# Optimization experiments

Measured on AMD Instinct MI355X. Metric: run time of the kernel, lower is better.

The kernel has to match this reference:

```python
import jax, jax.numpy as jnp
import numpy as np

N_QUBITS = 10
N_GEN = 4
Q_DEPTH = 6
BATCH = 1024


def _cz_chain_diag(n):
    # Diagonal of the CZ chain CZ(0,1) CZ(1,2) ... CZ(n-2,n-1):
    # phase (-1)^(# adjacent 1-1 pairs) per computational basis state.
    idx = np.arange(2 ** n)
    bits = (idx[:, None] >> np.arange(n - 1, -1, -1)) & 1  # wire 0 = most significant (PennyLane)
    pairs = (bits[:, :-1] & bits[:, 1:]).sum(axis=1)
    return ((-1.0) ** pairs).astype(np.float32).reshape((2,) * n)

_CZ = jnp.asarray(_cz_chain_diag(N_QUBITS))


def _ry(t):
    c = jnp.cos(0.5 * t)
    s = jnp.sin(0.5 * t)
    return jnp.stack([jnp.stack([c, -s]), jnp.stack([s, c])]).astype(jnp.complex64)


def _rx(t):
    c = jnp.cos(0.5 * t).astype(jnp.complex64)
    js = (1j * jnp.sin(0.5 * t)).astype(jnp.complex64)
    return jnp.stack([jnp.stack([c, -js]), jnp.stack([-js, c])])


def _apply_1q(state, gate, wire):
    # state: (2,)*n complex statevector; apply 2x2 gate on `wire`.
    state = jnp.moveaxis(state, wire, -1)
    state = jnp.einsum('...j,ij->...i', state, gate)
    return jnp.moveaxis(state, -1, wire)


def _circuit(noise_s, weights, cz):
    # noise_s: (n_qubits,), weights: (q_depth, n_qubits)
    n = noise_s.shape[0]
    state = jnp.zeros((2,) * n, jnp.complex64).at[(0,) * n].set(1.0)
    for q in range(n):
        state = _apply_1q(state, _ry(noise_s[q]), q)
        state = _apply_1q(state, _rx(noise_s[q]), q)

    def layer(st, w):
        for q in range(n):
            st = _apply_1q(st, _ry(w[q]), q)
        return st * cz, None

    state, _ = jax.lax.scan(layer, state, weights)
    # <X_q> = Re <psi| X_q |psi>; X_q flips the q-th wire.
    return jnp.stack([jnp.real(jnp.vdot(state, jnp.flip(state, axis=q))) for q in range(n)])


def setup_inputs() -> dict:
    key = jax.random.key(0)
    k1, k2 = jax.random.split(key)
    noise = jax.random.normal(k1, (BATCH, N_QUBITS), dtype=jnp.float32)
    q_params = jax.random.uniform(k2, (N_GEN, Q_DEPTH, N_QUBITS), dtype=jnp.float32)  # q_delta=1.0 * rand
    return {"noise": noise, "q_params": q_params}


def reference(noise, q_params):
    per_sample = lambda ns, w: _circuit(ns, w, _CZ)
    per_gen = jax.vmap(lambda w: jax.vmap(lambda ns: per_sample(ns, w))(noise))(q_params)  # (G, B, n)
    out = jnp.transpose(per_gen, (1, 0, 2)).reshape(noise.shape[0], N_GEN * N_QUBITS)
    return out.astype(jnp.float32)
```

## Files before the change

kernel.cpp:

```cpp
#include <hip/hip_runtime.h>

#define NQ 10
#define NG 4
#define QD 6
#define NBATCH 1024


template<int CTRL, int RM, int BM, bool BC>
__device__ __forceinline__ float dppmov(float x) {
    return __int_as_float(__builtin_amdgcn_update_dpp(
        0, __float_as_int(x), CTRL, RM, BM, BC));
}
template<int CTRL>
__device__ __forceinline__ float dpp1(float x) { return dppmov<CTRL,0xF,0xF,true>(x); }

template<int PAT>
__device__ __forceinline__ float swz(float x) {
    return __int_as_float(__builtin_amdgcn_ds_swizzle(__float_as_int(x), PAT));
}

struct FX1 { static __device__ __forceinline__ float f(float x){ return dpp1<0xB1>(x); } };
struct FX2 { static __device__ __forceinline__ float f(float x){ return dpp1<0x4E>(x); } };
struct FX4 { static __device__ __forceinline__ float f(float x){ return swz<0x101F>(x); } };
struct FX8 { static __device__ __forceinline__ float f(float x){ return swz<0x201F>(x); } };
struct FX16{ static __device__ __forceinline__ float f(float x){ return swz<0x401F>(x); } };
struct FX32{ static __device__ __forceinline__ float f(float x){ return __shfl_xor(x, 32, 64); } };

__device__ __forceinline__ float rlane(float v, int idx) {
    return __int_as_float(__builtin_amdgcn_readlane(__float_as_int(v), idx));
}

__device__ __forceinline__ float wave_reduce(float x) {
    x += dppmov<0x111,0xF,0xF,true >(x);
    x += dppmov<0x112,0xF,0xF,true >(x);
    x += dppmov<0x114,0xF,0xF,true >(x);
    x += dppmov<0x118,0xF,0xF,true >(x);
    x += dppmov<0x142,0xA,0xF,false>(x);
    x += dppmov<0x143,0xC,0xF,false>(x);
    return __int_as_float(__builtin_amdgcn_readlane(__float_as_int(x), 63));
}

__device__ __forceinline__ float wave_product(float x) {
    x *= dpp1<0xB1>(x);
    x *= dpp1<0x4E>(x);
    x *= FX4::f(x);
    x *= FX8::f(x);
    x *= FX16::f(x);
    x *= FX32::f(x);
    return x;
}

template<int M>
__device__ __forceinline__ void intra1(float (&s)[16], float t) {
#pragma unroll
    for (int j = 0; j < 16; ++j)
        if ((j & M) == 0) {
            const int k = j | M;
            float v0 = s[j], v1 = s[k];
            s[j] = fmaf(-t, v1, v0);
            s[k] = fmaf( t, v0, v1);
        }
}

template<class PF, int LM>
__device__ __forceinline__ void cross1(float (&s)[16], float t, int lane) {
    const float sv = (lane & LM) ? t : -t;
#pragma unroll
    for (int j = 0; j < 16; ++j)
        s[j] = fmaf(PF::f(s[j]), sv, s[j]);
}

template<int C1, int C2, int LM>
__device__ __forceinline__ void cross1_dpp2(float (&s)[16], float t, int lane) {
    const float sv = (lane & LM) ? t : -t;
#pragma unroll
    for (int j = 0; j < 16; ++j) {
        float tmp = dpp1<C1>(s[j]);
        s[j] = fmaf(dpp1<C2>(tmp), sv, s[j]);
    }
}

template<class PF>
__device__ __forceinline__ float cross_exp1(const float (&s)[16]) {
    float a = 0.f;
#pragma unroll
    for (int j = 0; j < 16; ++j)
        a = fmaf(PF::f(s[j]), s[j], a);
    return a;
}

template<int C1, int C2>
__device__ __forceinline__ float cross_exp_dpp2(const float (&s)[16]) {
    float a = 0.f;
#pragma unroll
    for (int j = 0; j < 16; ++j) {
        float tmp = dpp1<C1>(s[j]);
        a = fmaf(dpp1<C2>(tmp), s[j], a);
    }
    return a;
}

template<int M>
__device__ __forceinline__ float intra_exp1(const float (&s)[16]) {
    float a = 0.f;
#pragma unroll
    for (int j = 0; j < 16; ++j)
        a += s[j] * s[j ^ M];
    return a;
}

__global__ __launch_bounds__(256, 2) void qsim_kernel(
    const float* __restrict__ noise,
    const float* __restrict__ qp,
    float* __restrict__ out)
{
    __shared__ float partlds[2][16];

    const int wave = threadIdx.x >> 6;
    const int lane = threadIdx.x & 63;
    const int pc   = wave >> 1;
    const int comp = wave & 1;
    const int g    = blockIdx.x & 3;
    const int b    = (blockIdx.x >> 2) * 2 + pc;

    float wt, scale2;
    {
        const int widx = (lane < QD * NQ) ? lane : 0;
        float sv, cv;
        __sincosf(0.5f * qp[g * (QD * NQ) + widx], &sv, &cv);
        wt = sv / cv;
        float cvc = (lane < QD * NQ) ? cv : 1.0f;
        float p = wave_product(cvc);
        scale2 = p * p;
    }

    float s[16];
    {
        float nc[NQ], ns[NQ];
#pragma unroll
        for (int q = 0; q < NQ; ++q)
            __sincosf(0.5f * noise[b * NQ + q], &ns[q], &nc[q]);

        auto facr = [&](int q, int bit) { return bit ? nc[q]*ns[q] : nc[q]*nc[q]; };
        auto faci = [&](int q, int bit) { return bit ? -nc[q]*ns[q] : -ns[q]*ns[q]; };

        float hr = 1.f, hi = 0.f;
#pragma unroll
        for (int p = 4; p <= 9; ++p) {
            const int q = NQ - 1 - p, bit = (lane >> (p - 4)) & 1;
            float fr = facr(q, bit), fi = faci(q, bit);
            float tr = hr * fr - hi * fi;
            float ti = hr * fi + hi * fr;
            hr = tr; hi = ti;
        }
        float t01r[4], t01i[4], t23r[4], t23i[4];
#pragma unroll
        for (int a = 0; a < 4; ++a) {
            float f9r = facr(9, a & 1), f9i = faci(9, a & 1);
            float f8r = facr(8, (a >> 1) & 1), f8i = faci(8, (a >> 1) & 1);
            t01r[a] = f9r * f8r - f9i * f8i;
            t01i[a] = f9r * f8i + f9i * f8r;
            float f7r = facr(7, a & 1), f7i = faci(7, a & 1);
            float f6r = facr(6, (a >> 1) & 1), f6i = faci(6, (a >> 1) & 1);
            t23r[a] = f7r * f6r - f7i * f6i;
            t23i[a] = f7r * f6i + f7i * f6r;
        }
        float prer[4], prei[4];
#pragma unroll
        for (int a = 0; a < 4; ++a) {
            prer[a] = hr * t01r[a] - hi * t01i[a];
            prei[a] = hr * t01i[a] + hi * t01r[a];
        }
#pragma unroll
        for (int j = 0; j < 16; ++j) {
            const float re = prer[j & 3] * t23r[j >> 2] - prei[j & 3] * t23i[j >> 2];
            const float im = prer[j & 3] * t23i[j >> 2] + prei[j & 3] * t23r[j >> 2];
            s[j] = (comp == 0) ? re : im;
        }
    }

    unsigned aE, aO;
    {
        unsigned parA = (unsigned)(__popc(lane & (lane >> 1)) & 1) << 31;
        aE = parA;
        aO = parA ^ ((unsigned)(lane & 1) << 31);
    }
    auto czA = [&](float (&v)[16]) {
#pragma unroll
        for (int j = 0; j < 16; ++j) {
            const bool jp = (__popc(j & (j >> 1)) & 1) != 0;
            const unsigned base = (j & 8) ? aO : aE;
            const unsigned m = jp ? (base ^ 0x80000000u) : base;
            v[j] = __uint_as_float(__float_as_uint(v[j]) ^ m);
        }
    };

#pragma unroll 1
    for (int l = 0; l < QD; ++l) {
        float t[NQ];
#pragma unroll
        for (int q = 0; q < NQ; ++q) t[q] = rlane(wt, l * NQ + q);

        cross1<FX32,32>(s, t[0], lane);
        cross1<FX16,16>(s, t[1], lane);
        cross1_dpp2<0x141,0x140, 8>(s, t[2], lane);
        cross1_dpp2<0x141,0x1B,  4>(s, t[3], lane);
        intra1<1>(s, t[9]);
        intra1<2>(s, t[8]);
        intra1<4>(s, t[7]);
        intra1<8>(s, t[6]);
        cross1<FX1, 1>(s, t[5], lane);
        cross1<FX2, 2>(s, t[4], lane);
        czA(s);
    }

    float myp = 0.f;
    {
        float p0 = cross_exp1<FX32>(s);
        float p1 = cross_exp1<FX16>(s);
        float p2 = cross_exp_dpp2<0x141,0x140>(s);
        float p3 = cross_exp_dpp2<0x141,0x1B >(s);
        float p4 = cross_exp1<FX2>(s);
        float p5 = cross_exp1<FX1>(s);
        float p6 = intra_exp1<8>(s);
        float p7 = intra_exp1<4>(s);
        float p8 = intra_exp1<2>(s);
        float p9 = intra_exp1<1>(s);
        float e0 = wave_reduce(p0);
        float e1 = wave_reduce(p1);
        float e2 = wave_reduce(p2);
        float e3 = wave_reduce(p3);
        float e4 = wave_reduce(p4);
        float e5 = wave_reduce(p5);
        float e6 = wave_reduce(p6);
        float e7 = wave_reduce(p7);
        float e8 = wave_reduce(p8);
        float e9 = wave_reduce(p9);
        myp = (lane == 0) ? e0 : myp;
        myp = (lane == 1) ? e1 : myp;
        myp = (lane == 2) ? e2 : myp;
        myp = (lane == 3) ? e3 : myp;
        myp = (lane == 4) ? e4 : myp;
        myp = (lane == 5) ? e5 : myp;
        myp = (lane == 6) ? e6 : myp;
        myp = (lane == 7) ? e7 : myp;
        myp = (lane == 8) ? e8 : myp;
        myp = (lane == 9) ? e9 : myp;
    }

    if (comp == 0 && lane < NQ) partlds[pc][lane] = myp;
    __syncthreads();
    if (comp == 1 && lane < NQ)
        out[b * (NG * NQ) + g * NQ + lane] = (myp + partlds[pc][lane]) * scale2;
}

extern "C" void kernel_launch(void* const* d_in, const int* in_sizes, int n_in,
                              void* d_out, int out_size, void* d_ws, size_t ws_size,
                              hipStream_t stream) {
    const float* noise = (const float*)d_in[0];
    const float* qp    = (const float*)d_in[1];
    float* out = (float*)d_out;

    const int nblocks = (NBATCH * NG) / 2;
    qsim_kernel<<<nblocks, 256, 0, stream>>>(noise, qp, out);
}
```

Measured before the change: 85.11 us.

## Keep real and imaginary parts in one wave per circuit instead of two

Each wave now holds both the real and imaginary amplitude arrays for one (batch, generator) circuit, instead of splitting them across two waves that combine through shared memory. This halves the wave count, removes the LDS exchange and __syncthreads, and computes the setup trig once per circuit rather than twice. In exchange each wave does twice the gate work and needs twice the state registers, which may lower occupancy. It also gives more independent instructions per wave to hide DPP and swizzle latency.

```diff
diff --git a/kernel.cpp b/kernel.cpp
--- a/kernel.cpp
+++ b/kernel.cpp
@@ -114,14 +114,11 @@
     const float* __restrict__ qp,
     float* __restrict__ out)
 {
-    __shared__ float partlds[2][16];
-
     const int wave = threadIdx.x >> 6;
     const int lane = threadIdx.x & 63;
-    const int pc   = wave >> 1;
-    const int comp = wave & 1;
-    const int g    = blockIdx.x & 3;
-    const int b    = (blockIdx.x >> 2) * 2 + pc;
+    const int cid  = blockIdx.x * 4 + wave;
+    const int g    = cid & 3;
+    const int b    = cid >> 2;
 
     float wt, scale2;
     {
@@ -134,7 +131,7 @@
         scale2 = p * p;
     }
 
-    float s[16];
+    float sre[16], sim[16];
     {
         float nc[NQ], ns[NQ];
 #pragma unroll
@@ -173,9 +170,8 @@
         }
 #pragma unroll
         for (int j = 0; j < 16; ++j) {
-            const float re = prer[j & 3] * t23r[j >> 2] - prei[j & 3] * t23i[j >> 2];
-            const float im = prer[j & 3] * t23i[j >> 2] + prei[j & 3] * t23r[j >> 2];
-            s[j] = (comp == 0) ? re : im;
+            sre[j] = prer[j & 3] * t23r[j >> 2] - prei[j & 3] * t23i[j >> 2];
+            sim[j] = prer[j & 3] * t23i[j >> 2] + prei[j & 3] * t23r[j >> 2];
         }
     }
 
@@ -201,41 +197,47 @@
 #pragma unroll
         for (int q = 0; q < NQ; ++q) t[q] = rlane(wt, l * NQ + q);
 
-        cross1<FX32,32>(s, t[0], lane);
-        cross1<FX16,16>(s, t[1], lane);
-        cross1_dpp2<0x141,0x140, 8>(s, t[2], lane);
-        cross1_dpp2<0x141,0x1B,  4>(s, t[3], lane);
-        intra1<1>(s, t[9]);
-        intra1<2>(s, t[8]);
-        intra1<4>(s, t[7]);
-        intra1<8>(s, t[6]);
-        cross1<FX1, 1>(s, t[5], lane);
-        cross1<FX2, 2>(s, t[4], lane);
-        czA(s);
+        cross1<FX32,32>(sre, t[0], lane);
+        cross1<FX32,32>(sim, t[0], lane);
+        cross1<FX16,16>(sre, t[1], lane);
+        cross1<FX16,16>(sim, t[1], lane);
+        cross1_dpp2<0x141,0x140, 8>(sre, t[2], lane);
+        cross1_dpp2<0x141,0x140, 8>(sim, t[2], lane);
+        cross1_dpp2<0x141,0x1B,  4>(sre, t[3], lane);
+        cross1_dpp2<0x141,0x1B,  4>(sim, t[3], lane);
+        intra1<1>(sre, t[9]);  intra1<1>(sim, t[9]);
+        intra1<2>(sre, t[8]);  intra1<2>(sim, t[8]);
+        intra1<4>(sre, t[7]);  intra1<4>(sim, t[7]);
+        intra1<8>(sre, t[6]);  intra1<8>(sim, t[6]);
+        cross1<FX1, 1>(sre, t[5], lane);
+        cross1<FX1, 1>(sim, t[5], lane);
+        cross1<FX2, 2>(sre, t[4], lane);
+        cross1<FX2, 2>(sim, t[4], lane);
+        czA(sre); czA(sim);
     }
 
     float myp = 0.f;
     {
-        float p0 = cross_exp1<FX32>(s);
-        float p1 = cross_exp1<FX16>(s);
-        float p2 = cross_exp_dpp2<0x141,0x140>(s);
-        float p3 = cross_exp_dpp2<0x141,0x1B >(s);
-        float p4 = cross_exp1<FX2>(s);
-        float p5 = cross_exp1<FX1>(s);
-        float p6 = intra_exp1<8>(s);
-        float p7 = intra_exp1<4>(s);
-        float p8 = intra_exp1<2>(s);
-        float p9 = intra_exp1<1>(s);
-        float e0 = wave_reduce(p0);
-        float e1 = wave_reduce(p1);
-        float e2 = wave_reduce(p2);
-        float e3 = wave_reduce(p3);
-        float e4 = wave_reduce(p4);
-        float e5 = wave_reduce(p5);
-        float e6 = wave_reduce(p6);
-        float e7 = wave_reduce(p7);
-        float e8 = wave_reduce(p8);
-        float e9 = wave_reduce(p9);
+        float a0 = cross_exp1<FX32>(sre) + cross_exp1<FX32>(sim);
+        float a1 = cross_exp1<FX16>(sre) + cross_exp1<FX16>(sim);
+        float a2 = cross_exp_dpp2<0x141,0x140>(sre) + cross_exp_dpp2<0x141,0x140>(sim);
+        float a3 = cross_exp_dpp2<0x141,0x1B >(sre) + cross_exp_dpp2<0x141,0x1B >(sim);
+        float a4 = cross_exp1<FX2>(sre) + cross_exp1<FX2>(sim);
+        float a5 = cross_exp1<FX1>(sre) + cross_exp1<FX1>(sim);
+        float a6 = intra_exp1<8>(sre) + intra_exp1<8>(sim);
+        float a7 = intra_exp1<4>(sre) + intra_exp1<4>(sim);
+        float a8 = intra_exp1<2>(sre) + intra_exp1<2>(sim);
+        float a9 = intra_exp1<1>(sre) + intra_exp1<1>(sim);
+        float e0 = wave_reduce(a0);
+        float e1 = wave_reduce(a1);
+        float e2 = wave_reduce(a2);
+        float e3 = wave_reduce(a3);
+        float e4 = wave_reduce(a4);
+        float e5 = wave_reduce(a5);
+        float e6 = wave_reduce(a6);
+        float e7 = wave_reduce(a7);
+        float e8 = wave_reduce(a8);
+        float e9 = wave_reduce(a9);
         myp = (lane == 0) ? e0 : myp;
         myp = (lane == 1) ? e1 : myp;
         myp = (lane == 2) ? e2 : myp;
@@ -248,10 +250,8 @@
         myp = (lane == 9) ? e9 : myp;
     }
 
-    if (comp == 0 && lane < NQ) partlds[pc][lane] = myp;
-    __syncthreads();
-    if (comp == 1 && lane < NQ)
-        out[b * (NG * NQ) + g * NQ + lane] = (myp + partlds[pc][lane]) * scale2;
+    if (lane < NQ)
+        out[b * (NG * NQ) + g * NQ + lane] = myp * scale2;
 }
 
 extern "C" void kernel_launch(void* const* d_in, const int* in_sizes, int n_in,
@@ -261,6 +261,6 @@
     const float* qp    = (const float*)d_in[1];
     float* out = (float*)d_out;
 
-    const int nblocks = (NBATCH * NG) / 2;
+    const int nblocks = NBATCH;
     qsim_kernel<<<nblocks, 256, 0, stream>>>(noise, qp, out);
 }
```

Measured after the change: 84.38 us. No clear change (-0.9%).
